# Kernel optimization log

Hardware: AMD Instinct MI355X
Metric: run time of the kernel (lower is better)

## Reference

```python
import jax, jax.numpy as jnp
import numpy as np
import math

B, T, A, Z, E, H = 4, 16, 512, 512, 64, 8
HD = Z // H
NF = 6  # num Fourier freqs


def setup_inputs() -> dict:
    key = jax.random.key(0)
    ks = jax.random.split(key, 16)
    w = lambda k, shape: jax.random.normal(k, shape, jnp.float32) * 0.02
    return dict(
        z_current=jax.random.normal(ks[0], (B, A, Z), jnp.float32),
        z_pred=jax.random.normal(ks[1], (B, T, A, Z), jnp.float32),
        actions=jax.random.normal(ks[2], (B, T, 4), jnp.float32),
        Wq=w(ks[3], (Z, Z)), Wk=w(ks[4], (Z, Z)), Wv=w(ks[5], (Z, Z)),
        We=w(ks[6], (E, Z)), Wo=w(ks[7], (Z, Z)),
        g_lnq=jnp.ones((Z,), jnp.float32), b_lnq=jnp.zeros((Z,), jnp.float32),
        g_lno=jnp.ones((Z,), jnp.float32), b_lno=jnp.zeros((Z,), jnp.float32),
        W_ff1=w(ks[8], (Z, 4 * Z)), b_ff1=jnp.zeros((4 * Z,), jnp.float32),
        W_ff2=w(ks[9], (4 * Z, Z)), b_ff2=jnp.zeros((Z,), jnp.float32),
        W_edge=w(ks[10], (3 * 2 * NF + 2, E)), b_edge=jnp.zeros((E,), jnp.float32),
        Wg1=w(ks[11], (2 * Z, Z)), bg1=jnp.zeros((Z,), jnp.float32),
        Wg2=w(ks[12], (Z, 1)), bg2=jnp.zeros((1,), jnp.float32),
    )


def _ln(x, g, b, eps=1e-5):
    m = jnp.mean(x, -1, keepdims=True)
    v = jnp.var(x, -1, keepdims=True)
    return (x - m) * jax.lax.rsqrt(v + eps) * g + b


def _fourier(a3):
    # a3: [B,T,3] -> [B,T, 2 + 6*NF]
    dx, dy, th = a3[..., 0:1], a3[..., 1:2], a3[..., 2:3]
    feats = [jnp.sin(th), jnp.cos(th)]
    for k in range(NF):
        f = (2.0 ** k) * math.pi
        feats += [jnp.sin(f * dx), jnp.cos(f * dx),
                  jnp.sin(f * dy), jnp.cos(f * dy),
                  jnp.sin(f * th), jnp.cos(f * th)]
    return jnp.concatenate(feats, -1)


def reference(z_current, z_pred, actions, Wq, Wk, Wv, We, Wo,
              g_lnq, b_lnq, g_lno, b_lno, W_ff1, b_ff1, W_ff2, b_ff2,
              W_edge, b_edge, Wg1, bg1, Wg2, bg2):
    q = _ln(z_pred, g_lnq, b_lnq) @ Wq                      # [B,T,A,Z]
    kc = z_current @ Wk                                      # [B,A,Z]
    vc = z_current @ Wv                                      # [B,A,Z]
    e = (_fourier(actions[..., :3]) @ W_edge + b_edge) @ We  # [B,T,Z]
    k = kc[:, None, :, :] + e[:, :, None, :]                 # [B,T,A,Z] (edge-biased keys)

    qh = q.reshape(B, T, A, H, HD)
    kh = k.reshape(B, T, A, H, HD)
    vh = vc.reshape(B, A, H, HD)

    # Non-standard attention: outer product over head INDEX (i,j in [0,H)),
    # elementwise along head_dim d -> logits [B,T,A,HD,H,H]
    logits = jnp.einsum('btaid,btajd->btadij', qh, kh) / math.sqrt(HD)
    attn = jax.lax.stop_gradient(jax.nn.softmax(logits, axis=-1))  # torch @no_grad softmax
    out_h = jnp.einsum('btadij,bajd->btaid', attn, vh)       # [B,T,A,H,HD]
    out = out_h.reshape(B, T, A, Z) @ Wo

    gate_inp = jnp.concatenate([out, z_pred], -1)            # [B,T,A,2Z]
    g = jax.nn.sigmoid(
        jax.nn.gelu(gate_inp @ Wg1 + bg1, approximate=False) @ Wg2 + bg2)  # [B,T,A,1]

    z_mid = _ln(z_pred + g * out, g_lno, b_lno)
    return z_mid + (jax.nn.gelu(z_mid @ W_ff1 + b_ff1, approximate=False) @ W_ff2 + b_ff2)
```

## Files before the change

kernel.cpp:

```cpp
#include <hip/hip_runtime.h>
#include <hip/hip_bf16.h>
#include <math.h>


typedef __bf16 bf16x8 __attribute__((ext_vector_type(8)));
typedef float f32x4 __attribute__((ext_vector_type(4)));

#define ROWS 32768
#define ZDIM 512

__device__ __forceinline__ void gload16(const void* gptr, void* ldsptr) {
  __builtin_amdgcn_global_load_lds(
      (const __attribute__((address_space(1))) unsigned int*)gptr,
      (__attribute__((address_space(3))) unsigned int*)ldsptr, 16, 0, 0);
}

__device__ __forceinline__ float gelu_f(float x) {
  return 0.5f * x * (1.0f + erff(x * 0.70710678118654752f));
}

__global__ void transpose_f32_bf16(const float* __restrict__ in,
                                   __bf16* __restrict__ out, int R, int C) {
  __shared__ float tile[32][33];
  int c0 = blockIdx.x * 32, r0 = blockIdx.y * 32;
#pragma unroll
  for (int i = 0; i < 32; i += 8)
    tile[i + threadIdx.y][threadIdx.x] =
        in[(size_t)(r0 + i + threadIdx.y) * C + c0 + threadIdx.x];
  __syncthreads();
#pragma unroll
  for (int i = 0; i < 32; i += 8)
    out[(size_t)(c0 + i + threadIdx.y) * R + r0 + threadIdx.x] =
        (__bf16)tile[threadIdx.x][i + threadIdx.y];
}

__global__ void cvt_f32_bf16(const float* __restrict__ in,
                             __bf16* __restrict__ out) {
  int i = (blockIdx.x * 256 + threadIdx.x) * 4;
  float4 v = *(const float4*)(in + i);
  out[i + 0] = (__bf16)v.x;
  out[i + 1] = (__bf16)v.y;
  out[i + 2] = (__bf16)v.z;
  out[i + 3] = (__bf16)v.w;
}

template <bool GATED, bool EMIT_RAW>
__global__ __launch_bounds__(256) void ln_kernel(
    const float* __restrict__ xa, const __bf16* __restrict__ xb,
    const float* __restrict__ gate, const float* __restrict__ gamma,
    const float* __restrict__ beta, __bf16* __restrict__ out,
    __bf16* __restrict__ raw) {
  int row = blockIdx.x;
  int tid = threadIdx.x;
  int i0 = tid * 2;
  const float* ra = xa + (size_t)row * ZDIM;
  float x0 = ra[i0], x1 = ra[i0 + 1];
  if (EMIT_RAW) {
    raw[(size_t)row * ZDIM + i0] = (__bf16)x0;
    raw[(size_t)row * ZDIM + i0 + 1] = (__bf16)x1;
  }
  if (GATED) {
    float gv = gate[row];
    const __bf16* rb = xb + (size_t)row * ZDIM;
    x0 += gv * (float)rb[i0];
    x1 += gv * (float)rb[i0 + 1];
  }
  float s = x0 + x1, s2 = x0 * x0 + x1 * x1;
#pragma unroll
  for (int off = 32; off > 0; off >>= 1) {
    s += __shfl_down(s, off);
    s2 += __shfl_down(s2, off);
  }
  __shared__ float red[8];
  int wave = tid >> 6, lane = tid & 63;
  if (lane == 0) { red[wave] = s; red[4 + wave] = s2; }
  __syncthreads();
  float ts = red[0] + red[1] + red[2] + red[3];
  float ts2 = red[4] + red[5] + red[6] + red[7];
  float mean = ts * (1.0f / ZDIM);
  float var = ts2 * (1.0f / ZDIM) - mean * mean;
  float rstd = rsqrtf(var + 1e-5f);
  float y0 = (x0 - mean) * rstd * gamma[i0] + beta[i0];
  float y1 = (x1 - mean) * rstd * gamma[i0 + 1] + beta[i0 + 1];
  out[(size_t)row * ZDIM + i0] = (__bf16)y0;
  out[(size_t)row * ZDIM + i0 + 1] = (__bf16)y1;
}

__global__ void edge_kernel(const float* __restrict__ actions,
                            const float* __restrict__ W_edge,
                            const float* __restrict__ b_edge,
                            const float* __restrict__ We,
                            float* __restrict__ e) {
  int bt = blockIdx.x;
  int tid = threadIdx.x;
  float dx = actions[bt * 4 + 0];
  float dy = actions[bt * 4 + 1];
  float th = actions[bt * 4 + 2];
  float feats[38];
  feats[0] = sinf(th);
  feats[1] = cosf(th);
  int idx = 2;
  float f = 3.14159265358979323846f;
#pragma unroll
  for (int k = 0; k < 6; k++) {
    feats[idx++] = sinf(f * dx);
    feats[idx++] = cosf(f * dx);
    feats[idx++] = sinf(f * dy);
    feats[idx++] = cosf(f * dy);
    feats[idx++] = sinf(f * th);
    feats[idx++] = cosf(f * th);
    f *= 2.0f;
  }
  __shared__ float hid[64];
  float h = b_edge[tid];
  for (int ff = 0; ff < 38; ff++) h += feats[ff] * W_edge[ff * 64 + tid];
  hid[tid] = h;
  __syncthreads();
#pragma unroll
  for (int i = 0; i < 8; i++) {
    int z = i * 64 + tid;
    float sacc = 0.0f;
    for (int j = 0; j < 64; j++) sacc += hid[j] * We[j * ZDIM + z];
    e[(size_t)bt * ZDIM + z] = sacc;
  }
}

__global__ __launch_bounds__(256) void attn_kernel(
    const __bf16* __restrict__ q, const __bf16* __restrict__ kvc,
    const float* __restrict__ e, __bf16* __restrict__ attn_out) {
  int row = blockIdx.x * 4 + (threadIdx.x >> 6);
  int lane = threadIdx.x & 63;
  int a = row & 511;
  int bt = row >> 9;
  int b = bt >> 4;
  const __bf16* qr = q + (size_t)row * ZDIM;
  const __bf16* kr = kvc + ((size_t)b * 512 + a) * 1024;
  const __bf16* vr = kr + 512;
  const float* er = e + (size_t)bt * ZDIM;
  float kv[8], vv[8], qv[8];
#pragma unroll
  for (int j = 0; j < 8; j++) {
    kv[j] = (float)kr[j * 64 + lane] + er[j * 64 + lane];
    vv[j] = (float)vr[j * 64 + lane];
  }
#pragma unroll
  for (int i = 0; i < 8; i++) qv[i] = (float)qr[i * 64 + lane];
  const float scale = 0.125f;
#pragma unroll
  for (int i = 0; i < 8; i++) {
    float lg[8], m = -1e30f;
#pragma unroll
    for (int j = 0; j < 8; j++) {
      lg[j] = qv[i] * kv[j] * scale;
      m = fmaxf(m, lg[j]);
    }
    float ssum = 0.0f, o = 0.0f;
#pragma unroll
    for (int j = 0; j < 8; j++) {
      float p = __expf(lg[j] - m);
      ssum += p;
      o += p * vv[j];
    }
    attn_out[(size_t)row * ZDIM + i * 64 + lane] = (__bf16)(o / ssum);
  }
}

__global__ __launch_bounds__(256) void gate_kernel(
    const __bf16* __restrict__ hg, const float* __restrict__ Wg2,
    const float* __restrict__ bg2, float* __restrict__ g) {
  int row = blockIdx.x * 4 + (threadIdx.x >> 6);
  int lane = threadIdx.x & 63;
  float s = 0.0f;
#pragma unroll
  for (int i = 0; i < 8; i++) {
    int z = i * 64 + lane;
    s += (float)hg[(size_t)row * ZDIM + z] * Wg2[z];
  }
#pragma unroll
  for (int off = 32; off > 0; off >>= 1) s += __shfl_down(s, off);
  if (lane == 0) g[row] = 1.0f / (1.0f + expf(-(s + bg2[0])));
}

template <bool CONCAT, int EPI, typename OT>
__global__ __launch_bounds__(256) void gemm_kernel(
    const __bf16* __restrict__ A1, const __bf16* __restrict__ A2, int ksplit,
    int lda, const __bf16* __restrict__ Bt, const float* __restrict__ bias,
    const __bf16* __restrict__ resid, OT* __restrict__ C, int N, int K) {
  __shared__ __align__(16) __bf16 As[128 * 32];
  __shared__ __align__(16) __bf16 Bs[128 * 32];
  const int tid = threadIdx.x;
  const int wave = tid >> 6, lane = tid & 63;
  const int m0 = blockIdx.x * 128, n0 = blockIdx.y * 128;
  const int srow = lane >> 2;
  const int scol = (lane & 3) * 8;
  const int wm = (wave & 1) * 64, wn = (wave >> 1) * 64;
  const int fr = lane & 15, fq = lane >> 4;

  f32x4 acc[4][4] = {};

  for (int kt = 0; kt < K; kt += 32) {
    const __bf16* Ap;
    int ka;
    if (CONCAT) {
      if (kt < ksplit) { Ap = A1; ka = kt; }
      else             { Ap = A2; ka = kt - ksplit; }
    } else { Ap = A1; ka = kt; }
#pragma unroll
    for (int c = 0; c < 2; c++) {
      int r = 32 * wave + 16 * c + srow;
      gload16(Ap + (size_t)(m0 + r) * lda + ka + scol,
              &As[(32 * wave + 16 * c) * 32]);
      gload16(Bt + (size_t)(n0 + r) * K + kt + scol,
              &Bs[(32 * wave + 16 * c) * 32]);
    }
    __syncthreads();
    bf16x8 af[4], bfr[4];
#pragma unroll
    for (int t = 0; t < 4; t++) {
      af[t] = *(const bf16x8*)&As[(wm + t * 16 + fr) * 32 + fq * 8];
      bfr[t] = *(const bf16x8*)&Bs[(wn + t * 16 + fr) * 32 + fq * 8];
    }
#pragma unroll
    for (int mt = 0; mt < 4; mt++)
#pragma unroll
      for (int nt = 0; nt < 4; nt++)
        acc[mt][nt] = __builtin_amdgcn_mfma_f32_16x16x32_bf16(
            af[mt], bfr[nt], acc[mt][nt], 0, 0, 0);
    __syncthreads();
  }

#pragma unroll
  for (int mt = 0; mt < 4; mt++) {
#pragma unroll
    for (int nt = 0; nt < 4; nt++) {
      int col = n0 + wn + nt * 16 + fr;
#pragma unroll
      for (int r = 0; r < 4; r++) {
        int row = m0 + wm + mt * 16 + fq * 4 + r;
        float v = acc[mt][nt][r];
        if (EPI == 1) { v = gelu_f(v + bias[col]); }
        else if (EPI == 2) {
          v += bias[col] + (float)resid[(size_t)row * N + col];
        }
        C[(size_t)row * N + col] = (OT)v;
      }
    }
  }
}

extern "C" void kernel_launch(void* const* d_in, const int* in_sizes, int n_in,
                              void* d_out, int out_size, void* d_ws,
                              size_t ws_size, hipStream_t stream) {
  const float* z_current = (const float*)d_in[0];
  const float* z_pred = (const float*)d_in[1];
  const float* actions = (const float*)d_in[2];
  const float* Wq = (const float*)d_in[3];
  const float* Wk = (const float*)d_in[4];
  const float* Wv = (const float*)d_in[5];
  const float* We = (const float*)d_in[6];
  const float* Wo = (const float*)d_in[7];
  const float* g_lnq = (const float*)d_in[8];
  const float* b_lnq = (const float*)d_in[9];
  const float* g_lno = (const float*)d_in[10];
  const float* b_lno = (const float*)d_in[11];
  const float* W_ff1 = (const float*)d_in[12];
  const float* b_ff1 = (const float*)d_in[13];
  const float* W_ff2 = (const float*)d_in[14];
  const float* b_ff2 = (const float*)d_in[15];
  const float* W_edge = (const float*)d_in[16];
  const float* b_edge = (const float*)d_in[17];
  const float* Wg1 = (const float*)d_in[18];
  const float* bg1 = (const float*)d_in[19];
  const float* Wg2 = (const float*)d_in[20];
  const float* bg2 = (const float*)d_in[21];

  char* ws = (char*)d_ws;
  size_t off = 0;
  auto alloc = [&](size_t bytes) {
    void* p = ws + off;
    off += (bytes + 255) & ~(size_t)255;
    return p;
  };
  __bf16* WTkv = (__bf16*)alloc(1024 * 512 * 2);
  __bf16* WTq = (__bf16*)alloc(512 * 512 * 2);
  __bf16* WTo = (__bf16*)alloc(512 * 512 * 2);
  __bf16* WTg1 = (__bf16*)alloc(512 * 1024 * 2);
  __bf16* WTf1 = (__bf16*)alloc(2048 * 512 * 2);
  __bf16* WTf2 = (__bf16*)alloc(512 * 2048 * 2);
  __bf16* zc_bf = (__bf16*)alloc(2048 * 512 * 2);
  __bf16* zp_bf = (__bf16*)alloc((size_t)ROWS * ZDIM * 2);
  __bf16* kvc = (__bf16*)alloc(2048 * 1024 * 2);
  float* ebuf = (float*)alloc(64 * 512 * 4);
  float* gbuf = (float*)alloc(32768 * 4);
  __bf16* BUF_A = (__bf16*)alloc((size_t)2 * ROWS * ZDIM * 2);
  __bf16* BUF_B = BUF_A + (size_t)ROWS * ZDIM;
  __bf16* BUF_C = (__bf16*)alloc((size_t)ROWS * ZDIM * 2);
  (void)ws_size; (void)in_sizes; (void)n_in; (void)out_size;

  dim3 tb(32, 8);
  transpose_f32_bf16<<<dim3(16, 16), tb, 0, stream>>>(Wk, WTkv, 512, 512);
  transpose_f32_bf16<<<dim3(16, 16), tb, 0, stream>>>(Wv, WTkv + 512 * 512,
                                                      512, 512);
  transpose_f32_bf16<<<dim3(16, 16), tb, 0, stream>>>(Wq, WTq, 512, 512);
  transpose_f32_bf16<<<dim3(16, 16), tb, 0, stream>>>(Wo, WTo, 512, 512);
  transpose_f32_bf16<<<dim3(16, 32), tb, 0, stream>>>(Wg1, WTg1, 1024, 512);
  transpose_f32_bf16<<<dim3(64, 16), tb, 0, stream>>>(W_ff1, WTf1, 512, 2048);
  transpose_f32_bf16<<<dim3(16, 64), tb, 0, stream>>>(W_ff2, WTf2, 2048, 512);

  cvt_f32_bf16<<<1024, 256, 0, stream>>>(z_current, zc_bf);
  ln_kernel<false, true><<<ROWS, 256, 0, stream>>>(z_pred, nullptr, nullptr,
                                                   g_lnq, b_lnq, BUF_A, zp_bf);
  edge_kernel<<<64, 64, 0, stream>>>(actions, W_edge, b_edge, We, ebuf);
  gemm_kernel<false, 0, __bf16><<<dim3(16, 8), 256, 0, stream>>>(
      zc_bf, nullptr, 0, 512, WTkv, nullptr, nullptr, kvc, 1024, 512);
  gemm_kernel<false, 0, __bf16><<<dim3(256, 4), 256, 0, stream>>>(
      BUF_A, nullptr, 0, 512, WTq, nullptr, nullptr, BUF_B, 512, 512);
  attn_kernel<<<ROWS / 4, 256, 0, stream>>>(BUF_B, kvc, ebuf, BUF_A);
  gemm_kernel<false, 0, __bf16><<<dim3(256, 4), 256, 0, stream>>>(
      BUF_A, nullptr, 0, 512, WTo, nullptr, nullptr, BUF_B, 512, 512);
  gemm_kernel<true, 1, __bf16><<<dim3(256, 4), 256, 0, stream>>>(
      BUF_B, zp_bf, 512, 512, WTg1, bg1, nullptr, BUF_C, 512, 1024);
  gate_kernel<<<ROWS / 4, 256, 0, stream>>>(BUF_C, Wg2, bg2, gbuf);
  ln_kernel<true, false><<<ROWS, 256, 0, stream>>>(z_pred, BUF_B, gbuf, g_lno,
                                                   b_lno, BUF_C, nullptr);
  float* outp = (float*)d_out;
  __bf16* h1 = BUF_A;
  for (int c = 0; c < 2; c++) {
    const __bf16* zmid_c = BUF_C + (size_t)c * 16384 * 512;
    gemm_kernel<false, 1, __bf16><<<dim3(128, 16), 256, 0, stream>>>(
        zmid_c, nullptr, 0, 512, WTf1, b_ff1, nullptr, h1, 2048, 512);
    gemm_kernel<false, 2, float><<<dim3(128, 4), 256, 0, stream>>>(
        h1, nullptr, 0, 2048, WTf2, b_ff2, zmid_c,
        outp + (size_t)c * 16384 * 512, 512, 2048);
  }
}
```

Before: 749.5 us.

## Load GEMM fragments directly from global into registers with double buffering

The GEMM no longer stages A/B tiles in LDS. Each wave now loads its MFMA fragments straight from global memory into registers and ping-pongs between two register buffers so the next k-step's loads overlap the current MFMAs. MFMA sections are also wrapped in s_setprio. This removes the LDS round trip and both block barriers per k-step, but adds redundant global reads, since waves sharing rows or columns fetch the same data, and raises register pressure.

```diff
diff --git a/kernel.cpp b/kernel.cpp
--- a/kernel.cpp
+++ b/kernel.cpp
@@ -8,12 +8,6 @@
 
 #define ROWS 32768
 #define ZDIM 512
-
-__device__ __forceinline__ void gload16(const void* gptr, void* ldsptr) {
-  __builtin_amdgcn_global_load_lds(
-      (const __attribute__((address_space(1))) unsigned int*)gptr,
-      (__attribute__((address_space(3))) unsigned int*)ldsptr, 16, 0, 0);
-}
 
 __device__ __forceinline__ float gelu_f(float x) {
   return 0.5f * x * (1.0f + erff(x * 0.70710678118654752f));
@@ -186,48 +180,59 @@
     const __bf16* __restrict__ A1, const __bf16* __restrict__ A2, int ksplit,
     int lda, const __bf16* __restrict__ Bt, const float* __restrict__ bias,
     const __bf16* __restrict__ resid, OT* __restrict__ C, int N, int K) {
-  __shared__ __align__(16) __bf16 As[128 * 32];
-  __shared__ __align__(16) __bf16 Bs[128 * 32];
   const int tid = threadIdx.x;
   const int wave = tid >> 6, lane = tid & 63;
   const int m0 = blockIdx.x * 128, n0 = blockIdx.y * 128;
-  const int srow = lane >> 2;
-  const int scol = (lane & 3) * 8;
   const int wm = (wave & 1) * 64, wn = (wave >> 1) * 64;
   const int fr = lane & 15, fq = lane >> 4;
 
   f32x4 acc[4][4] = {};
 
-  for (int kt = 0; kt < K; kt += 32) {
+  const size_t arow = (size_t)(m0 + wm + fr) * lda + fq * 8;
+  const size_t brow = (size_t)(n0 + wn + fr) * K + fq * 8;
+
+  auto loadf = [&](bf16x8 af[4], bf16x8 bfr[4], int t) {
+    const int kt = t << 5;
     const __bf16* Ap;
     int ka;
     if (CONCAT) {
       if (kt < ksplit) { Ap = A1; ka = kt; }
       else             { Ap = A2; ka = kt - ksplit; }
     } else { Ap = A1; ka = kt; }
-#pragma unroll
-    for (int c = 0; c < 2; c++) {
-      int r = 32 * wave + 16 * c + srow;
-      gload16(Ap + (size_t)(m0 + r) * lda + ka + scol,
-              &As[(32 * wave + 16 * c) * 32]);
-      gload16(Bt + (size_t)(n0 + r) * K + kt + scol,
-              &Bs[(32 * wave + 16 * c) * 32]);
-    }
-    __syncthreads();
-    bf16x8 af[4], bfr[4];
-#pragma unroll
-    for (int t = 0; t < 4; t++) {
-      af[t] = *(const bf16x8*)&As[(wm + t * 16 + fr) * 32 + fq * 8];
-      bfr[t] = *(const bf16x8*)&Bs[(wn + t * 16 + fr) * 32 + fq * 8];
-    }
+    const __bf16* ab = Ap + arow + ka;
+    const __bf16* bb = Bt + brow + kt;
+#pragma unroll
+    for (int x = 0; x < 4; x++)
+      af[x] = *(const bf16x8*)(ab + (size_t)(x * 16) * lda);
+#pragma unroll
+    for (int x = 0; x < 4; x++)
+      bfr[x] = *(const bf16x8*)(bb + (size_t)(x * 16) * K);
+  };
+
+  auto mfmas = [&](bf16x8 af[4], bf16x8 bfr[4]) {
+    __builtin_amdgcn_s_setprio(1);
 #pragma unroll
     for (int mt = 0; mt < 4; mt++)
 #pragma unroll
       for (int nt = 0; nt < 4; nt++)
         acc[mt][nt] = __builtin_amdgcn_mfma_f32_16x16x32_bf16(
             af[mt], bfr[nt], acc[mt][nt], 0, 0, 0);
-    __syncthreads();
-  }
+    __builtin_amdgcn_s_setprio(0);
+  };
+
+  const int nk = K >> 5;
+  bf16x8 a0[4], b0[4], a1[4], b1[4];
+  loadf(a0, b0, 0);
+  int t = 0;
+  for (; t + 2 < nk; t += 2) {
+    loadf(a1, b1, t + 1);
+    mfmas(a0, b0);
+    loadf(a0, b0, t + 2);
+    mfmas(a1, b1);
+  }
+  loadf(a1, b1, t + 1);
+  mfmas(a0, b0);
+  mfmas(a1, b1);
 
 #pragma unroll
   for (int mt = 0; mt < 4; mt++) {
```

Measured after the change: 1.037 ms. 38.4% more time.
